# Performance work log

Measured on AMD Instinct MI355X. Metric: run time of the kernel, lower is better.

The kernel has to match this reference:

```python
import jax, jax.numpy as jnp
import numpy as np

KSIZE = 31
PAD = KSIZE // 2  # 15
SIGMA = 6.0
GAMMA_0 = 1.0
GAMMA_DELTA = 0.6
THRESH = 55.0


def _gabor_kernels(theta, freq):
    """Per-pixel spatially-varying Gabor kernels.
    theta, freq: [N] -> kernels [N, KSIZE, KSIZE].
    Frequency is chirped along the wave axis by freq_delta = freq/3 and the
    Gaussian aspect ratio varies from gamma_0 at the center by gamma_delta
    toward the kernel edge (matches generate_custom_gabor_torch semantics).
    """
    half = KSIZE // 2
    r = jnp.arange(-half, half + 1, dtype=jnp.float32)
    yy, xx = jnp.meshgrid(r, r, indexing='ij')  # [K,K]
    ct = jnp.cos(theta)[:, None, None]
    st = jnp.sin(theta)[:, None, None]
    x_t = xx * ct + yy * st       # along-wave coordinate
    y_t = -xx * st + yy * ct      # across-wave coordinate
    f0 = freq[:, None, None]
    f_local = f0 + (f0 / 3.0) * (y_t / half)          # freq_delta = freq/3
    gamma = GAMMA_0 + GAMMA_DELTA * jnp.abs(y_t) / half
    env = jnp.exp(-(x_t ** 2 + (gamma * y_t) ** 2) / (2.0 * SIGMA ** 2))
    return env * jnp.cos(2.0 * jnp.pi * f_local * x_t)


def _gabor_forward(fprint, freq_map, theta_map):
    H, W = fprint.shape
    i0, i1 = PAD, H - 16          # loop bounds: range(15, H-16)
    j0, j1 = PAD, W - 16
    Hout, Wout = i1 - i0, j1 - j0  # H-31, W-31 (patches always fully in-bounds)

    # [K*K, H-30, W-30] im2col patches; valid-output index 0 is center PAD.
    patches = jax.lax.conv_general_dilated_patches(
        fprint[None, None], (KSIZE, KSIZE), (1, 1), 'VALID')[0]
    patches = patches[:, :Hout, :Wout]  # centers i0..i1-1, j0..j1-1

    theta = theta_map[i0:i1, j0:j1].astype(jnp.float32) / 180.0 * jnp.pi
    freq = 0.025 + 0.0015 * freq_map[i0:i1, j0:j1].astype(jnp.float32)
    kernels = _gabor_kernels(theta.reshape(-1), freq.reshape(-1))
    kernels = kernels.reshape(Hout, Wout, KSIZE * KSIZE)

    vals = jnp.einsum('khw,hwk->hw', patches, kernels)
    out = fprint.at[i0:i1, j0:j1].set(vals)

    # normalize2Df_print_torch: shift min to 0, scale max to 100
    out = out - jnp.min(out)
    mx = jnp.max(out)
    out = jnp.where(mx != 0, out / mx * 100.0, out)
    # binarize2Df_print_torch
    return jnp.where(out > THRESH, 100.0, 0.0)


def setup_inputs() -> dict:
    key = jax.random.key(0)
    k1, k2, k3 = jax.random.split(key, 3)
    H = W = 320
    fprint = jax.random.uniform(k1, (H, W), dtype=jnp.float32) * 100.0
    freq_map = jax.random.randint(k2, (H, W), 0, 20, dtype=jnp.int32)
    theta_map = jax.random.randint(k3, (H, W), 0, 180, dtype=jnp.int32)
    return {"fprint": fprint, "freq_map": freq_map, "theta_map": theta_map}


def reference(fprint, freq_map, theta_map):
    return _gabor_forward(fprint, freq_map, theta_map)
```

## Files before the change

### kernel.cpp

```cpp
#include <hip/hip_runtime.h>
#include <math.h>

#define KS    31
#define KSP   32
#define PADV  15
#define IMG   320
#define NOUT  289
#define NTH   180
#define TABQ  (KSP * KSP)
#define RBLK  128

#define PBX   4
#define PBY   2
#define TROWS (PBY + KSP - 1)
#define TSTR  37
#define NSTG  (TROWS * TSTR)

typedef float f32x4 __attribute__((ext_vector_type(4)));

__global__ __launch_bounds__(256) void build_eftab(float2* __restrict__ tab) {
    const int t = blockIdx.x >> 2;
    const int e = (blockIdx.x & 3) * 256 + threadIdx.x;
    const float th = ((float)t / 180.0f) * 3.14159265358979323846f;
    float st, ct;
    sincosf(th, &st, &ct);
    int dy = e >> 5, dx = e & 31;
    float2 v = make_float2(0.0f, 0.0f);
    if (dy < KS && dx < KS) {
        float y = (float)(dy - PADV);
        float x = (float)(dx - PADV);
        float x_t = fmaf(x,  ct, y * st);
        float y_t = fmaf(-x, st, y * ct);
        float gamma = fmaf(0.04f, fabsf(y_t), 1.0f);
        float gyt = gamma * y_t;
        float env = expf(-fmaf(x_t, x_t, gyt * gyt) * (1.0f / 72.0f));
        float phi = fmaf(x_t * y_t, (1.0f / 45.0f), x_t);
        v = make_float2(env, phi);
    }
    tab[(size_t)t * TABQ + e] = v;
}

__global__ __launch_bounds__(256, 2) void gabor_conv(
    const float* __restrict__ fp, const int* __restrict__ fmap,
    const int* __restrict__ tmap, const float2* __restrict__ tab,
    float* __restrict__ out)
{
    __shared__ float tile[NSTG];
    const int bh = blockIdx.y * PBY;
    const int bw = blockIdx.x * PBX;
    const int tid = threadIdx.x;

    for (int i = tid; i < NSTG; i += 256) {
        int r = i / TSTR, c = i - r * TSTR;
        int gr = bh + r, gc = bw + c;
        tile[i] = (gr < IMG && gc < IMG) ? fp[gr * IMG + gc] : 0.0f;
    }
    __syncthreads();

    const int wave = tid >> 6, lane = tid & 63;
    const int half = lane >> 5, l = lane & 31;
    const int lr = l & 15, lh = l >> 4;
    const int pb  = wave * 2 + half;
    const int pxl = pb & 3, pyl = pb >> 2;
    const int oy = bh + pyl, ox = bw + pxl;
    const bool valid = (oy < NOUT) && (ox < NOUT);

    float acc0 = 0.0f, acc1 = 0.0f;
    if (valid) {
        const int iy = oy + PADV, ix = ox + PADV;
        const int theta = tmap[iy * IMG + ix];
        float f0 = 0.025f + 0.0015f * (float)fmap[iy * IMG + ix];
        asm volatile("" : "+v"(f0));

        unsigned long long a  =
            (unsigned long long)(tab + (size_t)theta * TABQ) + (size_t)l * 16;
        unsigned long long a2 = a + 4096;
        const float* tbase = &tile[(pyl + lh) * TSTR + pxl + 2 * lr];

        f32x4 g0a, g0b, g0c, g0d, g1a, g1b, g1c, g1d;
        f32x4 g2a, g2b, g2c, g2d, g3a, g3b, g3c, g3d;

#define ISSUE(R0,R1,R2,R3,A,O0,O1,O2,O3) asm volatile(                        \
        "global_load_dwordx4 %0, %4, off offset:" #O0 "\n\t"                  \
        "global_load_dwordx4 %1, %4, off offset:" #O1 "\n\t"                  \
        "global_load_dwordx4 %2, %4, off offset:" #O2 "\n\t"                  \
        "global_load_dwordx4 %3, %4, off offset:" #O3                         \
        : "=&v"(R0), "=&v"(R1), "=&v"(R2), "=&v"(R3) : "v"(A) : "memory")
#define WAITTIE(N,R0,R1,R2,R3)                                                \
        asm volatile("s_waitcnt vmcnt(" #N ")"                                \
            : "+v"(R0), "+v"(R1), "+v"(R2), "+v"(R3) :: "memory");            \
        __builtin_amdgcn_sched_barrier(0)
#define COMP(W, i) { const float* tr_ = tbase + 2 * (i) * TSTR;               \
        float w0_ = W.x * __builtin_amdgcn_cosf(f0 * W.y);                    \
        float w1_ = W.z * __builtin_amdgcn_cosf(f0 * W.w);                    \
        acc0 = fmaf(tr_[0], w0_, acc0); acc1 = fmaf(tr_[1], w1_, acc1); }

        ISSUE(g0a,g0b,g0c,g0d, a,  0,    512,  1024, 1536);
        ISSUE(g1a,g1b,g1c,g1d, a,  2048, 2560, 3072, 3584);
        WAITTIE(4, g0a,g0b,g0c,g0d);
        ISSUE(g2a,g2b,g2c,g2d, a2, 0,    512,  1024, 1536);
        COMP(g0a, 0) COMP(g0b, 1) COMP(g0c, 2) COMP(g0d, 3)
        __builtin_amdgcn_sched_barrier(0);
        WAITTIE(4, g1a,g1b,g1c,g1d);
        ISSUE(g3a,g3b,g3c,g3d, a2, 2048, 2560, 3072, 3584);
        COMP(g1a, 4) COMP(g1b, 5) COMP(g1c, 6) COMP(g1d, 7)
        __builtin_amdgcn_sched_barrier(0);
        WAITTIE(4, g2a,g2b,g2c,g2d);
        COMP(g2a, 8) COMP(g2b, 9) COMP(g2c, 10) COMP(g2d, 11)
        __builtin_amdgcn_sched_barrier(0);
        WAITTIE(0, g3a,g3b,g3c,g3d);
        COMP(g3a, 12) COMP(g3b, 13) COMP(g3c, 14) COMP(g3d, 15)
#undef COMP
#undef WAITTIE
#undef ISSUE
    }

    float v = acc0 + acc1;
    v += __shfl_xor(v, 1, 64);
    v += __shfl_xor(v, 2, 64);
    v += __shfl_xor(v, 4, 64);
    v += __shfl_xor(v, 8, 64);
    v += __shfl_xor(v, 16, 64);

    if (valid && l == 0)
        out[(oy + PADV) * IMG + (ox + PADV)] = v;
}

__global__ __launch_bounds__(256) void reduce_partials(
    const float* __restrict__ fp, const float* __restrict__ out,
    float2* __restrict__ part)
{
    __shared__ float smin[4], smax[4];
    float vmin = INFINITY, vmax = -INFINITY;
    for (int p = blockIdx.x * 256 + threadIdx.x; p < IMG * IMG; p += RBLK * 256) {
        int i = p / IMG, j = p - i * IMG;
        bool inner = (i >= PADV) && (i < PADV + NOUT) && (j >= PADV) && (j < PADV + NOUT);
        float v = inner ? out[p] : fp[p];
        vmin = fminf(vmin, v);
        vmax = fmaxf(vmax, v);
    }
    for (int off = 32; off; off >>= 1) {
        vmin = fminf(vmin, __shfl_down(vmin, off, 64));
        vmax = fmaxf(vmax, __shfl_down(vmax, off, 64));
    }
    const int wave = threadIdx.x >> 6;
    if ((threadIdx.x & 63) == 0) { smin[wave] = vmin; smax[wave] = vmax; }
    __syncthreads();
    if (threadIdx.x == 0) {
        vmin = fminf(fminf(smin[0], smin[1]), fminf(smin[2], smin[3]));
        vmax = fmaxf(fmaxf(smax[0], smax[1]), fmaxf(smax[2], smax[3]));
        part[blockIdx.x] = make_float2(vmin, vmax);
    }
}

__global__ __launch_bounds__(RBLK) void reduce_final(
    const float2* __restrict__ part, float* __restrict__ mm)
{
    __shared__ float smin[2], smax[2];
    float2 v = part[threadIdx.x];
    float vmin = v.x, vmax = v.y;
    for (int off = 32; off; off >>= 1) {
        vmin = fminf(vmin, __shfl_down(vmin, off, 64));
        vmax = fmaxf(vmax, __shfl_down(vmax, off, 64));
    }
    const int wave = threadIdx.x >> 6;
    if ((threadIdx.x & 63) == 0) { smin[wave] = vmin; smax[wave] = vmax; }
    __syncthreads();
    if (threadIdx.x == 0) {
        mm[0] = fminf(smin[0], smin[1]);
        mm[1] = fmaxf(smax[0], smax[1]);
    }
}

__global__ __launch_bounds__(256) void finalize(
    const float* __restrict__ fp, float* __restrict__ out,
    const float* __restrict__ mm)
{
    int p = blockIdx.x * 256 + threadIdx.x;
    if (p >= IMG * IMG) return;
    int i = p / IMG, j = p - i * IMG;
    bool inner = (i >= PADV) && (i < PADV + NOUT) && (j >= PADV) && (j < PADV + NOUT);
    float raw = inner ? out[p] : fp[p];
    float mn = mm[0];
    float mx = mm[1] - mn;
    float v  = raw - mn;
    if (mx != 0.0f) v = v / mx * 100.0f;
    out[p] = (v > 55.0f) ? 100.0f : 0.0f;
}

extern "C" void kernel_launch(void* const* d_in, const int* in_sizes, int n_in,
                              void* d_out, int out_size, void* d_ws, size_t ws_size,
                              hipStream_t stream) {
    const float* fp   = (const float*)d_in[0];
    const int*   fmap = (const int*)d_in[1];
    const int*   tmap = (const int*)d_in[2];
    float* out = (float*)d_out;

    float*  mm   = (float*)d_ws;
    float2* part = (float2*)((char*)d_ws + 256);
    float2* tab  = (float2*)((char*)d_ws + 4096);

    hipLaunchKernelGGL(build_eftab, dim3(NTH * 4), dim3(256), 0, stream, tab);

    dim3 g((NOUT + PBX - 1) / PBX, (NOUT + PBY - 1) / PBY);
    hipLaunchKernelGGL(gabor_conv, g, dim3(256), 0, stream, fp, fmap, tmap, tab, out);

    int nblk = (IMG * IMG + 255) / 256;
    hipLaunchKernelGGL(reduce_partials, dim3(RBLK), dim3(256), 0, stream, fp, out, part);
    hipLaunchKernelGGL(reduce_final,    dim3(1),    dim3(RBLK), 0, stream, part, mm);
    hipLaunchKernelGGL(finalize,        dim3(nblk), dim3(256), 0, stream, fp, out, mm);
}
```

Baseline: 44.96 us.

## Fuse per-block min/max into conv kernel and overlap table loads with tile staging

The conv kernel now writes a per-block min/max partial, so the separate full-image reduction pass is removed. A single 1024-thread final reduction combines the partials with the untouched border pixels. Table loads are issued before the shared-tile staging and barrier, so global latency overlaps the tile fill. Launch bounds are raised to 4 blocks per SM. The changes add a block barrier, about 10.6k partials to reduce in one block, and hardcoded border index arithmetic.

Result: slower. 51.61 us (+14.8%).

```diff
diff --git a/kernel.cpp b/kernel.cpp
--- a/kernel.cpp
+++ b/kernel.cpp
@@ -8,13 +8,16 @@
 #define NOUT  289
 #define NTH   180
 #define TABQ  (KSP * KSP)
-#define RBLK  128
 
 #define PBX   4
 #define PBY   2
 #define TROWS (PBY + KSP - 1)
 #define TSTR  37
 #define NSTG  (TROWS * TSTR)
+#define GX    73
+#define GY    145
+#define NPART (GX * GY)
+#define NBORD 18879
 
 typedef float f32x4 __attribute__((ext_vector_type(4)));
 
@@ -40,22 +43,16 @@
     tab[(size_t)t * TABQ + e] = v;
 }
 
-__global__ __launch_bounds__(256, 2) void gabor_conv(
+__global__ __launch_bounds__(256, 4) void gabor_conv(
     const float* __restrict__ fp, const int* __restrict__ fmap,
     const int* __restrict__ tmap, const float2* __restrict__ tab,
-    float* __restrict__ out)
+    float* __restrict__ out, float2* __restrict__ part)
 {
     __shared__ float tile[NSTG];
+    __shared__ float smin[8], smax[8];
     const int bh = blockIdx.y * PBY;
     const int bw = blockIdx.x * PBX;
     const int tid = threadIdx.x;
-
-    for (int i = tid; i < NSTG; i += 256) {
-        int r = i / TSTR, c = i - r * TSTR;
-        int gr = bh + r, gc = bw + c;
-        tile[i] = (gr < IMG && gc < IMG) ? fp[gr * IMG + gc] : 0.0f;
-    }
-    __syncthreads();
 
     const int wave = tid >> 6, lane = tid & 63;
     const int half = lane >> 5, l = lane & 31;
@@ -65,20 +62,10 @@
     const int oy = bh + pyl, ox = bw + pxl;
     const bool valid = (oy < NOUT) && (ox < NOUT);
 
-    float acc0 = 0.0f, acc1 = 0.0f;
-    if (valid) {
-        const int iy = oy + PADV, ix = ox + PADV;
-        const int theta = tmap[iy * IMG + ix];
-        float f0 = 0.025f + 0.0015f * (float)fmap[iy * IMG + ix];
-        asm volatile("" : "+v"(f0));
-
-        unsigned long long a  =
-            (unsigned long long)(tab + (size_t)theta * TABQ) + (size_t)l * 16;
-        unsigned long long a2 = a + 4096;
-        const float* tbase = &tile[(pyl + lh) * TSTR + pxl + 2 * lr];
-
-        f32x4 g0a, g0b, g0c, g0d, g1a, g1b, g1c, g1d;
-        f32x4 g2a, g2b, g2c, g2d, g3a, g3b, g3c, g3d;
+    f32x4 g0a, g0b, g0c, g0d, g1a, g1b, g1c, g1d;
+    f32x4 g2a, g2b, g2c, g2d, g3a, g3b, g3c, g3d;
+    float f0 = 0.0f;
+    unsigned long long a = 0;
 
 #define ISSUE(R0,R1,R2,R3,A,O0,O1,O2,O3) asm volatile(                        \
         "global_load_dwordx4 %0, %4, off offset:" #O0 "\n\t"                  \
@@ -90,19 +77,41 @@
         asm volatile("s_waitcnt vmcnt(" #N ")"                                \
             : "+v"(R0), "+v"(R1), "+v"(R2), "+v"(R3) :: "memory");            \
         __builtin_amdgcn_sched_barrier(0)
+#define WAITTIE8(R0,R1,R2,R3,R4,R5,R6,R7)                                     \
+        asm volatile("s_waitcnt vmcnt(8)"                                     \
+            : "+v"(R0), "+v"(R1), "+v"(R2), "+v"(R3),                         \
+              "+v"(R4), "+v"(R5), "+v"(R6), "+v"(R7) :: "memory");            \
+        __builtin_amdgcn_sched_barrier(0)
 #define COMP(W, i) { const float* tr_ = tbase + 2 * (i) * TSTR;               \
         float w0_ = W.x * __builtin_amdgcn_cosf(f0 * W.y);                    \
         float w1_ = W.z * __builtin_amdgcn_cosf(f0 * W.w);                    \
         acc0 = fmaf(tr_[0], w0_, acc0); acc1 = fmaf(tr_[1], w1_, acc1); }
 
-        ISSUE(g0a,g0b,g0c,g0d, a,  0,    512,  1024, 1536);
-        ISSUE(g1a,g1b,g1c,g1d, a,  2048, 2560, 3072, 3584);
-        WAITTIE(4, g0a,g0b,g0c,g0d);
+    if (valid) {
+        const int iy = oy + PADV, ix = ox + PADV;
+        const int theta = tmap[iy * IMG + ix];
+        f0 = 0.025f + 0.0015f * (float)fmap[iy * IMG + ix];
+        a = (unsigned long long)(tab + (size_t)theta * TABQ) + (size_t)l * 16;
+        ISSUE(g0a,g0b,g0c,g0d, a, 0,    512,  1024, 1536);
+        ISSUE(g1a,g1b,g1c,g1d, a, 2048, 2560, 3072, 3584);
+    }
+
+    for (int i = tid; i < NSTG; i += 256) {
+        int r = i / TSTR, c = i - r * TSTR;
+        int gr = bh + r, gc = bw + c;
+        tile[i] = (gr < IMG && gc < IMG) ? fp[gr * IMG + gc] : 0.0f;
+    }
+    __syncthreads();
+
+    float acc0 = 0.0f, acc1 = 0.0f;
+    if (valid) {
+        unsigned long long a2 = a + 4096;
+        const float* tbase = &tile[(pyl + lh) * TSTR + pxl + 2 * lr];
+
         ISSUE(g2a,g2b,g2c,g2d, a2, 0,    512,  1024, 1536);
+        ISSUE(g3a,g3b,g3c,g3d, a2, 2048, 2560, 3072, 3584);
+        WAITTIE8(g0a,g0b,g0c,g0d,g1a,g1b,g1c,g1d);
         COMP(g0a, 0) COMP(g0b, 1) COMP(g0c, 2) COMP(g0d, 3)
-        __builtin_amdgcn_sched_barrier(0);
-        WAITTIE(4, g1a,g1b,g1c,g1d);
-        ISSUE(g3a,g3b,g3c,g3d, a2, 2048, 2560, 3072, 3584);
         COMP(g1a, 4) COMP(g1b, 5) COMP(g1c, 6) COMP(g1d, 7)
         __builtin_amdgcn_sched_barrier(0);
         WAITTIE(4, g2a,g2b,g2c,g2d);
@@ -110,10 +119,11 @@
         __builtin_amdgcn_sched_barrier(0);
         WAITTIE(0, g3a,g3b,g3c,g3d);
         COMP(g3a, 12) COMP(g3b, 13) COMP(g3c, 14) COMP(g3d, 15)
+    }
 #undef COMP
+#undef WAITTIE8
 #undef WAITTIE
 #undef ISSUE
-    }
 
     float v = acc0 + acc1;
     v += __shfl_xor(v, 1, 64);
@@ -122,20 +132,48 @@
     v += __shfl_xor(v, 8, 64);
     v += __shfl_xor(v, 16, 64);
 
-    if (valid && l == 0)
-        out[(oy + PADV) * IMG + (ox + PADV)] = v;
-}
-
-__global__ __launch_bounds__(256) void reduce_partials(
-    const float* __restrict__ fp, const float* __restrict__ out,
-    float2* __restrict__ part)
+    if (l == 0) {
+        smin[pb] = valid ? v : INFINITY;
+        smax[pb] = valid ? v : -INFINITY;
+        if (valid) out[(oy + PADV) * IMG + (ox + PADV)] = v;
+    }
+    __syncthreads();
+    if (tid == 0) {
+        float mn = smin[0], mx = smax[0];
+        #pragma unroll
+        for (int k = 1; k < 8; ++k) {
+            mn = fminf(mn, smin[k]);
+            mx = fmaxf(mx, smax[k]);
+        }
+        part[blockIdx.y * GX + blockIdx.x] = make_float2(mn, mx);
+    }
+}
+
+__global__ __launch_bounds__(1024) void reduce_final(
+    const float2* __restrict__ part, const float* __restrict__ fp,
+    float* __restrict__ mm)
 {
-    __shared__ float smin[4], smax[4];
+    __shared__ float smin[16], smax[16];
     float vmin = INFINITY, vmax = -INFINITY;
-    for (int p = blockIdx.x * 256 + threadIdx.x; p < IMG * IMG; p += RBLK * 256) {
-        int i = p / IMG, j = p - i * IMG;
-        bool inner = (i >= PADV) && (i < PADV + NOUT) && (j >= PADV) && (j < PADV + NOUT);
-        float v = inner ? out[p] : fp[p];
+    for (int i = threadIdx.x; i < NPART; i += 1024) {
+        float2 p = part[i];
+        vmin = fminf(vmin, p.x);
+        vmax = fmaxf(vmax, p.y);
+    }
+    for (int t = threadIdx.x; t < NBORD; t += 1024) {
+        int p;
+        if (t < 4800) {
+            p = t;
+        } else if (t < 9920) {
+            int s = t - 4800;
+            p = (304 + s / 320) * 320 + (s % 320);
+        } else {
+            int s = t - 9920;
+            int r = 15 + s / 31, c = s % 31;
+            int col = (c < 15) ? c : 289 + c;
+            p = r * 320 + col;
+        }
+        float v = fp[p];
         vmin = fminf(vmin, v);
         vmax = fmaxf(vmax, v);
     }
@@ -147,28 +185,14 @@
     if ((threadIdx.x & 63) == 0) { smin[wave] = vmin; smax[wave] = vmax; }
     __syncthreads();
     if (threadIdx.x == 0) {
-        vmin = fminf(fminf(smin[0], smin[1]), fminf(smin[2], smin[3]));
-        vmax = fmaxf(fmaxf(smax[0], smax[1]), fmaxf(smax[2], smax[3]));
-        part[blockIdx.x] = make_float2(vmin, vmax);
-    }
-}
-
-__global__ __launch_bounds__(RBLK) void reduce_final(
-    const float2* __restrict__ part, float* __restrict__ mm)
-{
-    __shared__ float smin[2], smax[2];
-    float2 v = part[threadIdx.x];
-    float vmin = v.x, vmax = v.y;
-    for (int off = 32; off; off >>= 1) {
-        vmin = fminf(vmin, __shfl_down(vmin, off, 64));
-        vmax = fmaxf(vmax, __shfl_down(vmax, off, 64));
-    }
-    const int wave = threadIdx.x >> 6;
-    if ((threadIdx.x & 63) == 0) { smin[wave] = vmin; smax[wave] = vmax; }
-    __syncthreads();
-    if (threadIdx.x == 0) {
-        mm[0] = fminf(smin[0], smin[1]);
-        mm[1] = fmaxf(smax[0], smax[1]);
+        float mn = smin[0], mx = smax[0];
+        #pragma unroll
+        for (int k = 1; k < 16; ++k) {
+            mn = fminf(mn, smin[k]);
+            mx = fmaxf(mx, smax[k]);
+        }
+        mm[0] = mn;
+        mm[1] = mx;
     }
 }
 
@@ -198,15 +222,15 @@
 
     float*  mm   = (float*)d_ws;
     float2* part = (float2*)((char*)d_ws + 256);
-    float2* tab  = (float2*)((char*)d_ws + 4096);
+    float2* tab  = (float2*)((char*)d_ws + 131072);
 
     hipLaunchKernelGGL(build_eftab, dim3(NTH * 4), dim3(256), 0, stream, tab);
 
-    dim3 g((NOUT + PBX - 1) / PBX, (NOUT + PBY - 1) / PBY);
-    hipLaunchKernelGGL(gabor_conv, g, dim3(256), 0, stream, fp, fmap, tmap, tab, out);
+    hipLaunchKernelGGL(gabor_conv, dim3(GX, GY), dim3(256), 0, stream,
+                       fp, fmap, tmap, tab, out, part);
+
+    hipLaunchKernelGGL(reduce_final, dim3(1), dim3(1024), 0, stream, part, fp, mm);
 
     int nblk = (IMG * IMG + 255) / 256;
-    hipLaunchKernelGGL(reduce_partials, dim3(RBLK), dim3(256), 0, stream, fp, out, part);
-    hipLaunchKernelGGL(reduce_final,    dim3(1),    dim3(RBLK), 0, stream, part, mm);
-    hipLaunchKernelGGL(finalize,        dim3(nblk), dim3(256), 0, stream, fp, out, mm);
-}
+    hipLaunchKernelGGL(finalize, dim3(nblk), dim3(256), 0, stream, fp, out, mm);
+}
```
